# Kernel optimization log

Measured on AMD Instinct MI355X. Metric: run time of the kernel, lower is better.

## Reference

```python
import jax, jax.numpy as jnp
import numpy as np

BN_EPS = 1e-5

def _gin_mlp(h, wa, ba, wb, bb):
    # 2-layer MLP: Linear -> ReLU -> Linear
    return jax.nn.relu(h @ wa + ba) @ wb + bb

def _gin_conv(x, src, dst, n, wa, ba, wb, bb):
    # GIN aggregation: (1+eps)*x + sum_{j->i} x_j, eps=0 (PyG default)
    agg = jax.ops.segment_sum(x[src], dst, num_segments=n)
    return _gin_mlp(x + agg, wa, ba, wb, bb)

def _batchnorm(h, gamma, beta):
    # track_running_stats=False -> always batch stats, biased variance
    mean = jnp.mean(h, axis=0)
    var = jnp.var(h, axis=0)
    return (h - mean) * jax.lax.rsqrt(var + BN_EPS) * gamma + beta

def setup_inputs() -> dict:
    key = jax.random.key(0)
    ks = jax.random.split(key, 8)
    N, E, F, H, C = 100000, 1600000, 64, 64, 10
    s = 0.05
    return {
        "x": jax.random.normal(ks[0], (N, F), dtype=jnp.float32),
        "edge_index": jax.random.randint(ks[1], (2, E), 0, N, dtype=jnp.int64),
        "w1a": jax.random.normal(ks[2], (F, H), dtype=jnp.float32) * s,
        "b1a": jnp.zeros((H,), jnp.float32),
        "w1b": jax.random.normal(ks[3], (H, H), dtype=jnp.float32) * s,
        "b1b": jnp.zeros((H,), jnp.float32),
        "bn_gamma": jnp.ones((H,), jnp.float32),
        "bn_beta": jnp.zeros((H,), jnp.float32),
        "w2a": jax.random.normal(ks[4], (H, H), dtype=jnp.float32) * s,
        "b2a": jnp.zeros((H,), jnp.float32),
        "w2b": jax.random.normal(ks[5], (H, H), dtype=jnp.float32) * s,
        "b2b": jnp.zeros((H,), jnp.float32),
        "lin_w": jax.random.normal(ks[6], (H, C), dtype=jnp.float32) * s,
        "lin_b": jnp.zeros((C,), jnp.float32),
    }

def reference(x, edge_index, w1a, b1a, w1b, b1b, bn_gamma, bn_beta,
              w2a, b2a, w2b, b2b, lin_w, lin_b):
    n = x.shape[0]
    src, dst = edge_index[0], edge_index[1]
    h1 = _gin_conv(x, src, dst, n, w1a, b1a, w1b, b1b)   # [N, H]
    h1 = _batchnorm(h1, bn_gamma, bn_beta)               # relu1 never applied (faithful)
    h2 = _gin_conv(h1, src, dst, n, w2a, b2a, w2b, b2b)  # [N, H]
    return h2 @ lin_w + lin_b                            # [N, C]
```

## Files before the change

kernel.cpp:

```cpp
#include <hip/hip_runtime.h>
#include <hip/hip_fp16.h>

#define H 64
#define CBS 512
#define CB_BITS 9
#define TILE 8192
#define CAP 9216
#define NSTAT 64

typedef _Float16 f16;
typedef __attribute__((ext_vector_type(8))) _Float16 v8h;
typedef __attribute__((ext_vector_type(4))) float v4f;

__global__ __launch_bounds__(256)
void cvt_init_kernel(const float* __restrict__ x, f16* __restrict__ xh, int total4,
                     int* __restrict__ gcursor, int CB) {
    int i = blockIdx.x * blockDim.x + threadIdx.x;
    if (blockIdx.x == 0) {
        int t = threadIdx.x;
        if (t < CB) gcursor[t * 16] = t * CAP;
    }
    if (i >= total4) return;
    float4 v = ((const float4*)x)[i];
    f16 h0 = (f16)v.x, h1 = (f16)v.y, h2 = (f16)v.z, h3 = (f16)v.w;
    ushort4 pk;
    pk.x = *(unsigned short*)&h0; pk.y = *(unsigned short*)&h1;
    pk.z = *(unsigned short*)&h2; pk.w = *(unsigned short*)&h3;
    ((ushort4*)xh)[i] = pk;
}

__global__ __launch_bounds__(256)
void part_staged_kernel(const int* __restrict__ ei, int* __restrict__ gcursor,
                        int* __restrict__ pairs, int E, int N, int CB) {
    __shared__ int sd[256];
    __shared__ int excl[256];
    __shared__ int gbase[256];
    __shared__ int lcur[256];
    __shared__ int stage[TILE];
    __shared__ unsigned char bin8[TILE];
    int t = threadIdx.x;
    int ntiles = (E + TILE - 1) / TILE;
    for (int tile = blockIdx.x; tile < ntiles; tile += gridDim.x) {
        int base = tile * TILE;
        int cnt = min(TILE, E - base);
        sd[t] = 0;
        __syncthreads();
        for (int i = t; i < cnt; i += 256) {
            int s = ei[base + i];
            int d = ei[E + base + i];
            if ((unsigned)s < (unsigned)N && (unsigned)d < (unsigned)N)
                atomicAdd(&sd[d >> CB_BITS], 1);
        }
        __syncthreads();
        int v = sd[t];
        __syncthreads();
        for (int off = 1; off < 256; off <<= 1) {
            int add = (t >= off) ? sd[t - off] : 0;
            __syncthreads();
            sd[t] += add;
            __syncthreads();
        }
        int ex = sd[t] - v;
        excl[t] = ex;
        lcur[t] = ex;
        if (t < CB && v > 0) gbase[t] = atomicAdd(&gcursor[t * 16], v);
        int tot = sd[255];
        __syncthreads();
        for (int i = t; i < cnt; i += 256) {
            int s = ei[base + i];
            int d = ei[E + base + i];
            if ((unsigned)s < (unsigned)N && (unsigned)d < (unsigned)N) {
                int cb = d >> CB_BITS;
                int pos = atomicAdd(&lcur[cb], 1);
                stage[pos] = s | ((d & (CBS - 1)) << 17);
                bin8[pos] = (unsigned char)cb;
            }
        }
        __syncthreads();
        for (int i = t; i < tot; i += 256) {
            int b8 = bin8[i];
            pairs[gbase[b8] + (i - excl[b8])] = stage[i];
        }
        __syncthreads();
    }
}

__global__ __launch_bounds__(256)
void scan_cb_kernel(const int* __restrict__ gcursor, int* __restrict__ gbb,
                    int* __restrict__ rowptr, int CB, int N) {
    __shared__ int sd[256];
    int t = threadIdx.x;
    int cnt = (t < CB) ? (gcursor[t * 16] - t * CAP) : 0;
    sd[t] = cnt; __syncthreads();
    for (int off = 1; off < 256; off <<= 1) {
        int add = (t >= off) ? sd[t - off] : 0;
        __syncthreads();
        sd[t] += add;
        __syncthreads();
    }
    if (t < CB) gbb[t] = sd[t] - cnt;
    if (t == 0) { gbb[CB] = sd[255]; rowptr[N] = sd[255]; }
}

__global__ __launch_bounds__(256)
void bucket_csr_kernel(const int* __restrict__ pairs, const int* __restrict__ gcursor,
                       const int* __restrict__ gbb,
                       int* __restrict__ ebuf, int* __restrict__ rowptr, int N) {
    __shared__ int hist[CBS];
    __shared__ int cur[CBS];
    __shared__ int sd[256];
    __shared__ int carry_s;
    int b = blockIdx.x;
    int t = threadIdx.x;
    int pb = b * CAP;
    int cnt = gcursor[b * 16] - pb;
    int gb = gbb[b];
    for (int i = t; i < CBS; i += 256) hist[i] = 0;
    if (t == 0) carry_s = 0;
    __syncthreads();
    for (int i = t; i < cnt; i += 256)
        atomicAdd(&hist[(pairs[pb + i] >> 17) & (CBS - 1)], 1);
    __syncthreads();
    for (int start = 0; start < CBS; start += 256) {
        int v = hist[start + t];
        sd[t] = v; __syncthreads();
        for (int off = 1; off < 256; off <<= 1) {
            int add = (t >= off) ? sd[t - off] : 0;
            __syncthreads();
            sd[t] += add;
            __syncthreads();
        }
        int ex = sd[t] - v + carry_s;
        cur[start + t] = ex;
        int node = b * CBS + start + t;
        if (node < N) rowptr[node] = gb + ex;
        __syncthreads();
        if (t == 0) carry_s += sd[255];
        __syncthreads();
    }
    for (int i = t; i < cnt; i += 256) {
        int p = pairs[pb + i];
        int pos = atomicAdd(&cur[(p >> 17) & (CBS - 1)], 1);
        ebuf[gb + pos] = p & 0x1FFFF;
    }
}

__global__ void repack_kernel(const float* __restrict__ W1a, const float* __restrict__ W1b,
                              const float* __restrict__ W2a, const float* __restrict__ W2b,
                              const float* __restrict__ B2b, const float* __restrict__ LW,
                              const float* __restrict__ LB,
                              f16* __restrict__ pk1a, f16* __restrict__ pk1b,
                              f16* __restrict__ pk2a, f16* __restrict__ pkf,
                              float* __restrict__ bf, float* __restrict__ statsR) {
    int t = blockIdx.x * blockDim.x + threadIdx.x;
    if (t < NSTAT * 128) statsR[t] = 0.f;
    if (t < 12288) {
        int m = t >> 12;
        int e = t & 4095;
        int j = e & 7, lane = (e >> 3) & 63, ks = (e >> 9) & 1, nt = e >> 10;
        int row = ks * 32 + ((lane >> 4) & 3) * 8 + j;
        int col = nt * 16 + (lane & 15);
        const float* W = (m == 0) ? W1a : (m == 1) ? W1b : W2a;
        f16* P = (m == 0) ? pk1a : (m == 1) ? pk1b : pk2a;
        P[e] = (f16)W[row * 64 + col];
    } else if (t < 13312) {
        int e = t - 12288;
        int j = e & 7, lane = (e >> 3) & 63, ks = e >> 9;
        int row = ks * 32 + ((lane >> 4) & 3) * 8 + j;
        int col = lane & 15;
        float a = 0.f;
        if (col < 10)
            for (int m = 0; m < H; ++m) a = fmaf(W2b[row * 64 + m], LW[m * 10 + col], a);
        pkf[e] = (f16)a;
    } else if (t < 13322) {
        int c = t - 13312;
        float a = LB[c];
        for (int m = 0; m < H; ++m) a = fmaf(B2b[m], LW[m * 10 + c], a);
        bf[c] = a;
    }
}

__global__ __launch_bounds__(256)
void gather1_kernel(const f16* __restrict__ xh, const int* __restrict__ rowptr,
                    const int* __restrict__ ebuf, f16* __restrict__ bufA,
                    int N, int Em1) {
    int wid = (int)(((long long)blockIdx.x * blockDim.x + threadIdx.x) >> 6);
    int lane = threadIdx.x & 63;
    int g = lane >> 3, fl = lane & 7;
    int node = wid * 8 + g;
    bool vn = node < N;
    int p0 = 0, deg = 0;
    if (vn) {
        p0 = rowptr[node];
        deg = rowptr[node + 1] - p0;
    }
    int m = deg;
    m = max(m, __shfl_xor(m, 8));
    m = max(m, __shfl_xor(m, 16));
    m = max(m, __shfl_xor(m, 32));

    float a[8];
    {
        v8h s = {};
        if (vn) s = *(const v8h*)(xh + ((size_t)node << 6) + fl * 8);
#pragma unroll
        for (int j = 0; j < 8; ++j) a[j] = (float)s[j];
    }
    for (int k = 0; k < m; k += 4) {
        int idx[4];
#pragma unroll
        for (int q = 0; q < 4; ++q)
            idx[q] = ebuf[min(p0 + k + q, Em1)];
#pragma unroll
        for (int q = 0; q < 4; ++q) {
            if (k + q < deg) {
                v8h v = *(const v8h*)(xh + ((size_t)idx[q] << 6) + fl * 8);
#pragma unroll
                for (int j = 0; j < 8; ++j) a[j] += (float)v[j];
            }
        }
    }
    if (vn) {
        v8h o;
#pragma unroll
        for (int j = 0; j < 8; ++j) o[j] = (f16)a[j];
        *(v8h*)(bufA + ((size_t)node << 6) + fl * 8) = o;
    }
}

__global__ __launch_bounds__(256)
void gather2_kernel(const f16* __restrict__ h1p, const float* __restrict__ scale,
                    const float* __restrict__ shiftv, const int* __restrict__ rowptr,
                    const int* __restrict__ ebuf, f16* __restrict__ bufC,
                    int N, int Em1) {
    int wid = (int)(((long long)blockIdx.x * blockDim.x + threadIdx.x) >> 6);
    int lane = threadIdx.x & 63;
    int g = lane >> 3, fl = lane & 7;
    int node = wid * 8 + g;
    bool vn = node < N;
    int p0 = 0, deg = 0;
    if (vn) {
        p0 = rowptr[node];
        deg = rowptr[node + 1] - p0;
    }
    int m = deg;
    m = max(m, __shfl_xor(m, 8));
    m = max(m, __shfl_xor(m, 16));
    m = max(m, __shfl_xor(m, 32));

    float a[8];
    {
        v8h s = {};
        if (vn) s = *(const v8h*)(h1p + ((size_t)node << 6) + fl * 8);
#pragma unroll
        for (int j = 0; j < 8; ++j) a[j] = (float)s[j];
    }
    for (int k = 0; k < m; k += 4) {
        int idx[4];
#pragma unroll
        for (int q = 0; q < 4; ++q)
            idx[q] = ebuf[min(p0 + k + q, Em1)];
#pragma unroll
        for (int q = 0; q < 4; ++q) {
            if (k + q < deg) {
                v8h v = *(const v8h*)(h1p + ((size_t)idx[q] << 6) + fl * 8);
#pragma unroll
                for (int j = 0; j < 8; ++j) a[j] += (float)v[j];
            }
        }
    }
    if (vn) {
        float4 sc0 = *(const float4*)(scale + fl * 8);
        float4 sc1 = *(const float4*)(scale + fl * 8 + 4);
        float4 sh0 = *(const float4*)(shiftv + fl * 8);
        float4 sh1 = *(const float4*)(shiftv + fl * 8 + 4);
        float degp1 = (float)(deg + 1);
        float sc[8] = {sc0.x, sc0.y, sc0.z, sc0.w, sc1.x, sc1.y, sc1.z, sc1.w};
        float sh[8] = {sh0.x, sh0.y, sh0.z, sh0.w, sh1.x, sh1.y, sh1.z, sh1.w};
        v8h o;
#pragma unroll
        for (int j = 0; j < 8; ++j) o[j] = (f16)(a[j] * sc[j] + degp1 * sh[j]);
        *(v8h*)(bufC + ((size_t)node << 6) + fl * 8) = o;
    }
}

__global__ __launch_bounds__(256)
void mlp1_kernel(const f16* __restrict__ bufA, f16* __restrict__ h1p,
                 const f16* __restrict__ pk1a, const f16* __restrict__ pk1b,
                 const float* __restrict__ B1a, const float* __restrict__ B1b,
                 float* __restrict__ statsR, int N) {
    __shared__ f16 Su[4][16 * 72];
    __shared__ f16 Sh[4][16 * 72];
    __shared__ float red[2][4][64];
    int t = threadIdx.x, wv = t >> 6, lane = t & 63;
    int quad = lane >> 4, r16 = lane & 15;
    int node0 = blockIdx.x * 64 + wv * 16;
    int nodeA = node0 + r16;

    v8h a0 = {}, a1 = {};
    if (nodeA < N) {
        a0 = *(const v8h*)(bufA + (size_t)nodeA * 64 + quad * 8);
        a1 = *(const v8h*)(bufA + (size_t)nodeA * 64 + 32 + quad * 8);
    }
#pragma unroll
    for (int nt = 0; nt < 4; ++nt) {
        v8h b0 = *(const v8h*)(pk1a + (((nt * 2 + 0) * 64 + lane) << 3));
        v8h b1 = *(const v8h*)(pk1a + (((nt * 2 + 1) * 64 + lane) << 3));
        v4f c = {0.f, 0.f, 0.f, 0.f};
        c = __builtin_amdgcn_mfma_f32_16x16x32_f16(a0, b0, c, 0, 0, 0);
        c = __builtin_amdgcn_mfma_f32_16x16x32_f16(a1, b1, c, 0, 0, 0);
        float bias = B1a[nt * 16 + r16];
#pragma unroll
        for (int reg = 0; reg < 4; ++reg)
            Su[wv][(quad * 4 + reg) * 72 + nt * 16 + r16] = (f16)fmaxf(c[reg] + bias, 0.f);
    }
    __syncthreads();
    v8h u0 = *(const v8h*)(&Su[wv][r16 * 72 + quad * 8]);
    v8h u1 = *(const v8h*)(&Su[wv][r16 * 72 + 32 + quad * 8]);
#pragma unroll
    for (int nt = 0; nt < 4; ++nt) {
        v8h b0 = *(const v8h*)(pk1b + (((nt * 2 + 0) * 64 + lane) << 3));
        v8h b1 = *(const v8h*)(pk1b + (((nt * 2 + 1) * 64 + lane) << 3));
        v4f c = {0.f, 0.f, 0.f, 0.f};
        c = __builtin_amdgcn_mfma_f32_16x16x32_f16(u0, b0, c, 0, 0, 0);
        c = __builtin_amdgcn_mfma_f32_16x16x32_f16(u1, b1, c, 0, 0, 0);
        float bias = B1b[nt * 16 + r16];
#pragma unroll
        for (int reg = 0; reg < 4; ++reg) {
            int row = quad * 4 + reg;
            bool valid = (node0 + row) < N;
            Sh[wv][row * 72 + nt * 16 + r16] = valid ? (f16)(c[reg] + bias) : (f16)0;
        }
    }
    __syncthreads();
    for (int i = lane; i < 1024; i += 64) {
        int row = i >> 6, col = i & 63;
        int node = node0 + row;
        if (node < N) h1p[(size_t)node * 64 + col] = Sh[wv][row * 72 + col];
    }
    float s = 0.f, s2 = 0.f;
#pragma unroll
    for (int row = 0; row < 16; ++row) {
        float v = (float)Sh[wv][row * 72 + lane];
        s += v;
        s2 = fmaf(v, v, s2);
    }
    red[0][wv][lane] = s;
    red[1][wv][lane] = s2;
    __syncthreads();
    if (wv == 0) {
        float ts  = (red[0][0][lane] + red[0][1][lane]) + (red[0][2][lane] + red[0][3][lane]);
        float ts2 = (red[1][0][lane] + red[1][1][lane]) + (red[1][2][lane] + red[1][3][lane]);
        float* st = statsR + (size_t)(blockIdx.x & (NSTAT - 1)) * 128;
        unsafeAtomicAdd(&st[lane], ts);
        unsafeAtomicAdd(&st[64 + lane], ts2);
    }
}

__global__ void bn_finalize_kernel(const float* __restrict__ statsR,
                                   const float* __restrict__ gamma,
                                   const float* __restrict__ beta,
                                   float* __restrict__ scale, float* __restrict__ shiftv, float n) {
    int f = threadIdx.x;
    if (f >= H) return;
    float s = 0.f, s2 = 0.f;
    for (int r = 0; r < NSTAT; ++r) {
        s  += statsR[r * 128 + f];
        s2 += statsR[r * 128 + 64 + f];
    }
    float mean = s / n;
    float var = s2 / n - mean * mean;
    var = fmaxf(var, 0.f);
    float sc = gamma[f] * rsqrtf(var + 1e-5f);
    scale[f] = sc;
    shiftv[f] = beta[f] - mean * sc;
}

__global__ __launch_bounds__(256)
void mlp2_kernel(const f16* __restrict__ bufC,
                 const f16* __restrict__ pk2a, const f16* __restrict__ pkf,
                 const float* __restrict__ B2a, const float* __restrict__ bf,
                 float* __restrict__ out, int N) {
    __shared__ f16 Su[4][16 * 72];
    int t = threadIdx.x, wv = t >> 6, lane = t & 63;
    int quad = lane >> 4, r16 = lane & 15;
    int node0 = blockIdx.x * 64 + wv * 16;
    int nodeA = node0 + r16;

    v8h a0 = {}, a1 = {};
    if (nodeA < N) {
        a0 = *(const v8h*)(bufC + (size_t)nodeA * 64 + quad * 8);
        a1 = *(const v8h*)(bufC + (size_t)nodeA * 64 + 32 + quad * 8);
    }
#pragma unroll
    for (int nt = 0; nt < 4; ++nt) {
        v8h b0 = *(const v8h*)(pk2a + (((nt * 2 + 0) * 64 + lane) << 3));
        v8h b1 = *(const v8h*)(pk2a + (((nt * 2 + 1) * 64 + lane) << 3));
        v4f c = {0.f, 0.f, 0.f, 0.f};
        c = __builtin_amdgcn_mfma_f32_16x16x32_f16(a0, b0, c, 0, 0, 0);
        c = __builtin_amdgcn_mfma_f32_16x16x32_f16(a1, b1, c, 0, 0, 0);
        float bias = B2a[nt * 16 + r16];
#pragma unroll
        for (int reg = 0; reg < 4; ++reg)
            Su[wv][(quad * 4 + reg) * 72 + nt * 16 + r16] = (f16)fmaxf(c[reg] + bias, 0.f);
    }
    __syncthreads();
    v8h u0 = *(const v8h*)(&Su[wv][r16 * 72 + quad * 8]);
    v8h u1 = *(const v8h*)(&Su[wv][r16 * 72 + 32 + quad * 8]);
    v8h b0 = *(const v8h*)(pkf + ((0 * 64 + lane) << 3));
    v8h b1 = *(const v8h*)(pkf + ((1 * 64 + lane) << 3));
    v4f c = {0.f, 0.f, 0.f, 0.f};
    c = __builtin_amdgcn_mfma_f32_16x16x32_f16(u0, b0, c, 0, 0, 0);
    c = __builtin_amdgcn_mfma_f32_16x16x32_f16(u1, b1, c, 0, 0, 0);
    if (r16 < 10) {
        float bias = bf[r16];
#pragma unroll
        for (int reg = 0; reg < 4; ++reg) {
            int node = node0 + quad * 4 + reg;
            if (node < N) out[(size_t)node * 10 + r16] = c[reg] + bias;
        }
    }
}

extern "C" void kernel_launch(void* const* d_in, const int* in_sizes, int n_in,
                              void* d_out, int out_size, void* d_ws, size_t ws_size,
                              hipStream_t stream) {
    const float* x    = (const float*)d_in[0];
    const int*   ei   = (const int*)d_in[1];
    const float* w1a  = (const float*)d_in[2];
    const float* b1a  = (const float*)d_in[3];
    const float* w1b  = (const float*)d_in[4];
    const float* b1b  = (const float*)d_in[5];
    const float* bng  = (const float*)d_in[6];
    const float* bnb  = (const float*)d_in[7];
    const float* w2a  = (const float*)d_in[8];
    const float* b2a  = (const float*)d_in[9];
    const float* w2b  = (const float*)d_in[10];
    const float* b2b  = (const float*)d_in[11];
    const float* linw = (const float*)d_in[12];
    const float* linb = (const float*)d_in[13];

    int N = in_sizes[0] / H;
    int E = in_sizes[1] / 2;
    int CB = (N + CBS - 1) / CBS;

    size_t NH = (size_t)N * H;
    char*  wsb    = (char*)d_ws;
    f16*   xh     = (f16*)wsb;
    f16*   bufA   = (f16*)(wsb + NH * 2);
    f16*   bufC   = (f16*)(wsb + NH * 4);
    float* stats  = (float*)(wsb + NH * 6);
    float* scale  = stats + 128;
    float* shiftv = stats + 192;
    float* bf     = stats + 256;
    f16*   pk1a   = (f16*)(bf + 16);
    f16*   pk1b   = pk1a + 4096;
    f16*   pk2a   = pk1b + 4096;
    f16*   pkf    = pk2a + 4096;
    int*   gcursor= (int*)(pkf + 1024);
    int*   gbb    = gcursor + 256 * 16;
    int*   rowptr = gbb + 257;
    int*   ebuf   = rowptr + (N + 1);
    int*   pairs  = ebuf + E;
    float* statsR = (float*)pairs;

    int ntiles = (E + TILE - 1) / TILE;

    cvt_init_kernel<<<(int)((NH / 4 + 255) / 256), 256, 0, stream>>>(
        x, xh, (int)(NH / 4), gcursor, CB);
    part_staged_kernel<<<ntiles, 256, 0, stream>>>(ei, gcursor, pairs, E, N, CB);
    scan_cb_kernel<<<1, 256, 0, stream>>>(gcursor, gbb, rowptr, CB, N);
    bucket_csr_kernel<<<CB, 256, 0, stream>>>(pairs, gcursor, gbb, ebuf, rowptr, N);
    repack_kernel<<<(13322 + 255) / 256, 256, 0, stream>>>(
        w1a, w1b, w2a, w2b, b2b, linw, linb, pk1a, pk1b, pk2a, pkf, bf, statsR);

    int nwaves = (N + 7) / 8;
    int gblocks = (int)(((long long)nwaves * 64 + 255) / 256);
    int mblocks = (N + 63) / 64;
    gather1_kernel<<<gblocks, 256, 0, stream>>>(xh, rowptr, ebuf, bufA, N, E - 1);
    mlp1_kernel<<<mblocks, 256, 0, stream>>>(bufA, bufA, pk1a, pk1b, b1a, b1b, statsR, N);
    bn_finalize_kernel<<<1, 64, 0, stream>>>(statsR, bng, bnb, scale, shiftv, (float)N);

    gather2_kernel<<<gblocks, 256, 0, stream>>>(bufA, scale, shiftv, rowptr, ebuf, bufC, N, E - 1);
    mlp2_kernel<<<mblocks, 256, 0, stream>>>(bufC, pk2a, pkf, b2a, bf, (float*)d_out, N);
}
```

Baseline: 247.9 us.

## Fuse gathers into MLP kernels and merge front-end preprocessing kernels

Each neighbor-aggregation gather is fused into its following MFMA MLP kernel, so aggregated features stay in shared memory instead of going through a global buffer. The fp16 conversion, edge partitioning and weight repacking become one front kernel with block-range dispatch, and the bucket-count scan moves into every bucket_csr block. This removes several launches and a full N×64 write and read per layer. In exchange the fused kernels use more shared memory and registers, which may lower occupancy for the latency-bound gathers, and the scan is repeated in every block.

```diff
diff --git a/kernel.cpp b/kernel.cpp
--- a/kernel.cpp
+++ b/kernel.cpp
@@ -7,41 +7,41 @@
 #define TILE 8192
 #define CAP 9216
 #define NSTAT 64
+#define RPK_BLKS 53
 
 typedef _Float16 f16;
 typedef __attribute__((ext_vector_type(8))) _Float16 v8h;
 typedef __attribute__((ext_vector_type(4))) float v4f;
 
 __global__ __launch_bounds__(256)
-void cvt_init_kernel(const float* __restrict__ x, f16* __restrict__ xh, int total4,
-                     int* __restrict__ gcursor, int CB) {
-    int i = blockIdx.x * blockDim.x + threadIdx.x;
-    if (blockIdx.x == 0) {
-        int t = threadIdx.x;
-        if (t < CB) gcursor[t * 16] = t * CAP;
-    }
-    if (i >= total4) return;
-    float4 v = ((const float4*)x)[i];
-    f16 h0 = (f16)v.x, h1 = (f16)v.y, h2 = (f16)v.z, h3 = (f16)v.w;
-    ushort4 pk;
-    pk.x = *(unsigned short*)&h0; pk.y = *(unsigned short*)&h1;
-    pk.z = *(unsigned short*)&h2; pk.w = *(unsigned short*)&h3;
-    ((ushort4*)xh)[i] = pk;
+void init_kernel(int* __restrict__ gcursor, float* __restrict__ statsR, int CB) {
+    int t = threadIdx.x;
+    if (t < CB) gcursor[t * 16] = t * CAP;
+    for (int i = t; i < NSTAT * 128; i += 256) statsR[i] = 0.f;
 }
 
 __global__ __launch_bounds__(256)
-void part_staged_kernel(const int* __restrict__ ei, int* __restrict__ gcursor,
-                        int* __restrict__ pairs, int E, int N, int CB) {
+void front_kernel(const int* __restrict__ ei, int* __restrict__ gcursor,
+                  int* __restrict__ pairs, int E, int N, int CB, int ntiles,
+                  const float* __restrict__ x, f16* __restrict__ xh, int total4,
+                  const float* __restrict__ W1a, const float* __restrict__ W1b,
+                  const float* __restrict__ W2a, const float* __restrict__ W2b,
+                  const float* __restrict__ B2b, const float* __restrict__ LW,
+                  const float* __restrict__ LB,
+                  f16* __restrict__ pk1a, f16* __restrict__ pk1b,
+                  f16* __restrict__ pk2a, f16* __restrict__ pkf,
+                  float* __restrict__ bf) {
     __shared__ int sd[256];
     __shared__ int excl[256];
     __shared__ int gbase[256];
     __shared__ int lcur[256];
     __shared__ int stage[TILE];
     __shared__ unsigned char bin8[TILE];
+    int b = blockIdx.x;
     int t = threadIdx.x;
-    int ntiles = (E + TILE - 1) / TILE;
-    for (int tile = blockIdx.x; tile < ntiles; tile += gridDim.x) {
-        int base = tile * TILE;
+
+    if (b < ntiles) {
+        int base = b * TILE;
         int cnt = min(TILE, E - base);
         sd[t] = 0;
         __syncthreads();
@@ -81,40 +81,71 @@
             int b8 = bin8[i];
             pairs[gbase[b8] + (i - excl[b8])] = stage[i];
         }
-        __syncthreads();
-    }
-}
-
-__global__ __launch_bounds__(256)
-void scan_cb_kernel(const int* __restrict__ gcursor, int* __restrict__ gbb,
-                    int* __restrict__ rowptr, int CB, int N) {
-    __shared__ int sd[256];
-    int t = threadIdx.x;
-    int cnt = (t < CB) ? (gcursor[t * 16] - t * CAP) : 0;
-    sd[t] = cnt; __syncthreads();
-    for (int off = 1; off < 256; off <<= 1) {
-        int add = (t >= off) ? sd[t - off] : 0;
-        __syncthreads();
-        sd[t] += add;
-        __syncthreads();
-    }
-    if (t < CB) gbb[t] = sd[t] - cnt;
-    if (t == 0) { gbb[CB] = sd[255]; rowptr[N] = sd[255]; }
+        return;
+    }
+    b -= ntiles;
+    if (b < RPK_BLKS) {
+        int tt = b * 256 + t;
+        if (tt < 12288) {
+            int m = tt >> 12;
+            int e = tt & 4095;
+            int j = e & 7, lane = (e >> 3) & 63, ks = (e >> 9) & 1, nt = e >> 10;
+            int row = ks * 32 + ((lane >> 4) & 3) * 8 + j;
+            int col = nt * 16 + (lane & 15);
+            const float* W = (m == 0) ? W1a : (m == 1) ? W1b : W2a;
+            f16* P = (m == 0) ? pk1a : (m == 1) ? pk1b : pk2a;
+            P[e] = (f16)W[row * 64 + col];
+        } else if (tt < 13312) {
+            int e = tt - 12288;
+            int j = e & 7, lane = (e >> 3) & 63, ks = e >> 9;
+            int row = ks * 32 + ((lane >> 4) & 3) * 8 + j;
+            int col = lane & 15;
+            float a = 0.f;
+            if (col < 10)
+                for (int m = 0; m < H; ++m) a = fmaf(W2b[row * 64 + m], LW[m * 10 + col], a);
+            pkf[e] = (f16)a;
+        } else if (tt < 13322) {
+            int c = tt - 13312;
+            float a = LB[c];
+            for (int m = 0; m < H; ++m) a = fmaf(B2b[m], LW[m * 10 + c], a);
+            bf[c] = a;
+        }
+        return;
+    }
+    b -= RPK_BLKS;
+    int i = b * 256 + t;
+    if (i >= total4) return;
+    float4 v = ((const float4*)x)[i];
+    f16 h0 = (f16)v.x, h1 = (f16)v.y, h2 = (f16)v.z, h3 = (f16)v.w;
+    ushort4 pk;
+    pk.x = *(unsigned short*)&h0; pk.y = *(unsigned short*)&h1;
+    pk.z = *(unsigned short*)&h2; pk.w = *(unsigned short*)&h3;
+    ((ushort4*)xh)[i] = pk;
 }
 
 __global__ __launch_bounds__(256)
 void bucket_csr_kernel(const int* __restrict__ pairs, const int* __restrict__ gcursor,
-                       const int* __restrict__ gbb,
-                       int* __restrict__ ebuf, int* __restrict__ rowptr, int N) {
+                       int* __restrict__ ebuf, int* __restrict__ rowptr, int N, int CB) {
     __shared__ int hist[CBS];
     __shared__ int cur[CBS];
     __shared__ int sd[256];
     __shared__ int carry_s;
     int b = blockIdx.x;
     int t = threadIdx.x;
+    int c_t = (t < CB) ? (gcursor[t * 16] - t * CAP) : 0;
+    sd[t] = c_t; __syncthreads();
+    for (int off = 1; off < 256; off <<= 1) {
+        int add = (t >= off) ? sd[t - off] : 0;
+        __syncthreads();
+        sd[t] += add;
+        __syncthreads();
+    }
+    int cnt = gcursor[b * 16] - b * CAP;
+    int gb = sd[b] - cnt;
+    if (b == 0 && t == 0) rowptr[N] = sd[255];
+    __syncthreads();
+
     int pb = b * CAP;
-    int cnt = gcursor[b * 16] - pb;
-    int gb = gbb[b];
     for (int i = t; i < CBS; i += 256) hist[i] = 0;
     if (t == 0) carry_s = 0;
     __syncthreads();
@@ -145,163 +176,66 @@
     }
 }
 
-__global__ void repack_kernel(const float* __restrict__ W1a, const float* __restrict__ W1b,
-                              const float* __restrict__ W2a, const float* __restrict__ W2b,
-                              const float* __restrict__ B2b, const float* __restrict__ LW,
-                              const float* __restrict__ LB,
-                              f16* __restrict__ pk1a, f16* __restrict__ pk1b,
-                              f16* __restrict__ pk2a, f16* __restrict__ pkf,
-                              float* __restrict__ bf, float* __restrict__ statsR) {
-    int t = blockIdx.x * blockDim.x + threadIdx.x;
-    if (t < NSTAT * 128) statsR[t] = 0.f;
-    if (t < 12288) {
-        int m = t >> 12;
-        int e = t & 4095;
-        int j = e & 7, lane = (e >> 3) & 63, ks = (e >> 9) & 1, nt = e >> 10;
-        int row = ks * 32 + ((lane >> 4) & 3) * 8 + j;
-        int col = nt * 16 + (lane & 15);
-        const float* W = (m == 0) ? W1a : (m == 1) ? W1b : W2a;
-        f16* P = (m == 0) ? pk1a : (m == 1) ? pk1b : pk2a;
-        P[e] = (f16)W[row * 64 + col];
-    } else if (t < 13312) {
-        int e = t - 12288;
-        int j = e & 7, lane = (e >> 3) & 63, ks = e >> 9;
-        int row = ks * 32 + ((lane >> 4) & 3) * 8 + j;
-        int col = lane & 15;
-        float a = 0.f;
-        if (col < 10)
-            for (int m = 0; m < H; ++m) a = fmaf(W2b[row * 64 + m], LW[m * 10 + col], a);
-        pkf[e] = (f16)a;
-    } else if (t < 13322) {
-        int c = t - 13312;
-        float a = LB[c];
-        for (int m = 0; m < H; ++m) a = fmaf(B2b[m], LW[m * 10 + c], a);
-        bf[c] = a;
-    }
-}
-
 __global__ __launch_bounds__(256)
-void gather1_kernel(const f16* __restrict__ xh, const int* __restrict__ rowptr,
-                    const int* __restrict__ ebuf, f16* __restrict__ bufA,
-                    int N, int Em1) {
-    int wid = (int)(((long long)blockIdx.x * blockDim.x + threadIdx.x) >> 6);
-    int lane = threadIdx.x & 63;
-    int g = lane >> 3, fl = lane & 7;
-    int node = wid * 8 + g;
-    bool vn = node < N;
-    int p0 = 0, deg = 0;
-    if (vn) {
-        p0 = rowptr[node];
-        deg = rowptr[node + 1] - p0;
-    }
-    int m = deg;
-    m = max(m, __shfl_xor(m, 8));
-    m = max(m, __shfl_xor(m, 16));
-    m = max(m, __shfl_xor(m, 32));
-
-    float a[8];
-    {
-        v8h s = {};
-        if (vn) s = *(const v8h*)(xh + ((size_t)node << 6) + fl * 8);
-#pragma unroll
-        for (int j = 0; j < 8; ++j) a[j] = (float)s[j];
-    }
-    for (int k = 0; k < m; k += 4) {
-        int idx[4];
-#pragma unroll
-        for (int q = 0; q < 4; ++q)
-            idx[q] = ebuf[min(p0 + k + q, Em1)];
-#pragma unroll
-        for (int q = 0; q < 4; ++q) {
-            if (k + q < deg) {
-                v8h v = *(const v8h*)(xh + ((size_t)idx[q] << 6) + fl * 8);
-#pragma unroll
-                for (int j = 0; j < 8; ++j) a[j] += (float)v[j];
-            }
-        }
-    }
-    if (vn) {
-        v8h o;
-#pragma unroll
-        for (int j = 0; j < 8; ++j) o[j] = (f16)a[j];
-        *(v8h*)(bufA + ((size_t)node << 6) + fl * 8) = o;
-    }
-}
-
-__global__ __launch_bounds__(256)
-void gather2_kernel(const f16* __restrict__ h1p, const float* __restrict__ scale,
-                    const float* __restrict__ shiftv, const int* __restrict__ rowptr,
-                    const int* __restrict__ ebuf, f16* __restrict__ bufC,
-                    int N, int Em1) {
-    int wid = (int)(((long long)blockIdx.x * blockDim.x + threadIdx.x) >> 6);
-    int lane = threadIdx.x & 63;
-    int g = lane >> 3, fl = lane & 7;
-    int node = wid * 8 + g;
-    bool vn = node < N;
-    int p0 = 0, deg = 0;
-    if (vn) {
-        p0 = rowptr[node];
-        deg = rowptr[node + 1] - p0;
-    }
-    int m = deg;
-    m = max(m, __shfl_xor(m, 8));
-    m = max(m, __shfl_xor(m, 16));
-    m = max(m, __shfl_xor(m, 32));
-
-    float a[8];
-    {
-        v8h s = {};
-        if (vn) s = *(const v8h*)(h1p + ((size_t)node << 6) + fl * 8);
-#pragma unroll
-        for (int j = 0; j < 8; ++j) a[j] = (float)s[j];
-    }
-    for (int k = 0; k < m; k += 4) {
-        int idx[4];
-#pragma unroll
-        for (int q = 0; q < 4; ++q)
-            idx[q] = ebuf[min(p0 + k + q, Em1)];
-#pragma unroll
-        for (int q = 0; q < 4; ++q) {
-            if (k + q < deg) {
-                v8h v = *(const v8h*)(h1p + ((size_t)idx[q] << 6) + fl * 8);
-#pragma unroll
-                for (int j = 0; j < 8; ++j) a[j] += (float)v[j];
-            }
-        }
-    }
-    if (vn) {
-        float4 sc0 = *(const float4*)(scale + fl * 8);
-        float4 sc1 = *(const float4*)(scale + fl * 8 + 4);
-        float4 sh0 = *(const float4*)(shiftv + fl * 8);
-        float4 sh1 = *(const float4*)(shiftv + fl * 8 + 4);
-        float degp1 = (float)(deg + 1);
-        float sc[8] = {sc0.x, sc0.y, sc0.z, sc0.w, sc1.x, sc1.y, sc1.z, sc1.w};
-        float sh[8] = {sh0.x, sh0.y, sh0.z, sh0.w, sh1.x, sh1.y, sh1.z, sh1.w};
-        v8h o;
-#pragma unroll
-        for (int j = 0; j < 8; ++j) o[j] = (f16)(a[j] * sc[j] + degp1 * sh[j]);
-        *(v8h*)(bufC + ((size_t)node << 6) + fl * 8) = o;
-    }
-}
-
-__global__ __launch_bounds__(256)
-void mlp1_kernel(const f16* __restrict__ bufA, f16* __restrict__ h1p,
-                 const f16* __restrict__ pk1a, const f16* __restrict__ pk1b,
-                 const float* __restrict__ B1a, const float* __restrict__ B1b,
-                 float* __restrict__ statsR, int N) {
+void g1mlp1_kernel(const f16* __restrict__ xh, const int* __restrict__ rowptr,
+                   const int* __restrict__ ebuf, f16* __restrict__ h1p,
+                   const f16* __restrict__ pk1a, const f16* __restrict__ pk1b,
+                   const float* __restrict__ B1a, const float* __restrict__ B1b,
+                   float* __restrict__ statsR, int N, int Em1) {
+    __shared__ f16 agg[64][72];
     __shared__ f16 Su[4][16 * 72];
     __shared__ f16 Sh[4][16 * 72];
     __shared__ float red[2][4][64];
     int t = threadIdx.x, wv = t >> 6, lane = t & 63;
+    int g = lane >> 3, fl = lane & 7;
+    int node0 = blockIdx.x * 64;
+
+#pragma unroll
+    for (int r = 0; r < 2; ++r) {
+        int nl = wv * 16 + r * 8 + g;
+        int node = node0 + nl;
+        bool vn = node < N;
+        int p0 = 0, deg = 0;
+        if (vn) {
+            p0 = rowptr[node];
+            deg = rowptr[node + 1] - p0;
+        }
+        int m = deg;
+        m = max(m, __shfl_xor(m, 8));
+        m = max(m, __shfl_xor(m, 16));
+        m = max(m, __shfl_xor(m, 32));
+        float a[8];
+        {
+            v8h s = {};
+            if (vn) s = *(const v8h*)(xh + ((size_t)node << 6) + fl * 8);
+#pragma unroll
+            for (int j = 0; j < 8; ++j) a[j] = (float)s[j];
+        }
+        for (int k = 0; k < m; k += 4) {
+            int idx[4];
+#pragma unroll
+            for (int q = 0; q < 4; ++q)
+                idx[q] = ebuf[min(p0 + k + q, Em1)];
+#pragma unroll
+            for (int q = 0; q < 4; ++q) {
+                if (k + q < deg) {
+                    v8h v = *(const v8h*)(xh + ((size_t)idx[q] << 6) + fl * 8);
+#pragma unroll
+                    for (int j = 0; j < 8; ++j) a[j] += (float)v[j];
+                }
+            }
+        }
+        v8h o;
+#pragma unroll
+        for (int j = 0; j < 8; ++j) o[j] = (f16)a[j];
+        *(v8h*)(&agg[nl][fl * 8]) = o;
+    }
+    __syncthreads();
+
     int quad = lane >> 4, r16 = lane & 15;
-    int node0 = blockIdx.x * 64 + wv * 16;
-    int nodeA = node0 + r16;
-
-    v8h a0 = {}, a1 = {};
-    if (nodeA < N) {
-        a0 = *(const v8h*)(bufA + (size_t)nodeA * 64 + quad * 8);
-        a1 = *(const v8h*)(bufA + (size_t)nodeA * 64 + 32 + quad * 8);
-    }
+    int nodeA_l = wv * 16 + r16;
+    v8h a0 = *(const v8h*)(&agg[nodeA_l][quad * 8]);
+    v8h a1 = *(const v8h*)(&agg[nodeA_l][32 + quad * 8]);
 #pragma unroll
     for (int nt = 0; nt < 4; ++nt) {
         v8h b0 = *(const v8h*)(pk1a + (((nt * 2 + 0) * 64 + lane) << 3));
@@ -328,14 +262,15 @@
 #pragma unroll
         for (int reg = 0; reg < 4; ++reg) {
             int row = quad * 4 + reg;
-            bool valid = (node0 + row) < N;
+            bool valid = (node0 + wv * 16 + row) < N;
             Sh[wv][row * 72 + nt * 16 + r16] = valid ? (f16)(c[reg] + bias) : (f16)0;
         }
     }
     __syncthreads();
+    int nbase = node0 + wv * 16;
     for (int i = lane; i < 1024; i += 64) {
         int row = i >> 6, col = i & 63;
-        int node = node0 + row;
+        int node = nbase + row;
         if (node < N) h1p[(size_t)node * 64 + col] = Sh[wv][row * 72 + col];
     }
     float s = 0.f, s2 = 0.f;
@@ -377,21 +312,77 @@
 }
 
 __global__ __launch_bounds__(256)
-void mlp2_kernel(const f16* __restrict__ bufC,
-                 const f16* __restrict__ pk2a, const f16* __restrict__ pkf,
-                 const float* __restrict__ B2a, const float* __restrict__ bf,
-                 float* __restrict__ out, int N) {
+void g2mlp2_kernel(const f16* __restrict__ h1p, const float* __restrict__ scale,
+                   const float* __restrict__ shiftv, const int* __restrict__ rowptr,
+                   const int* __restrict__ ebuf,
+                   const f16* __restrict__ pk2a, const f16* __restrict__ pkf,
+                   const float* __restrict__ B2a, const float* __restrict__ bf,
+                   float* __restrict__ out, int N, int Em1) {
+    __shared__ f16 agg[64][72];
     __shared__ f16 Su[4][16 * 72];
     int t = threadIdx.x, wv = t >> 6, lane = t & 63;
+    int g = lane >> 3, fl = lane & 7;
+    int node0 = blockIdx.x * 64;
+
+    float sc[8], sh[8];
+    {
+        float4 s0 = *(const float4*)(scale + fl * 8);
+        float4 s1 = *(const float4*)(scale + fl * 8 + 4);
+        float4 h0 = *(const float4*)(shiftv + fl * 8);
+        float4 h1 = *(const float4*)(shiftv + fl * 8 + 4);
+        sc[0]=s0.x; sc[1]=s0.y; sc[2]=s0.z; sc[3]=s0.w;
+        sc[4]=s1.x; sc[5]=s1.y; sc[6]=s1.z; sc[7]=s1.w;
+        sh[0]=h0.x; sh[1]=h0.y; sh[2]=h0.z; sh[3]=h0.w;
+        sh[4]=h1.x; sh[5]=h1.y; sh[6]=h1.z; sh[7]=h1.w;
+    }
+
+#pragma unroll
+    for (int r = 0; r < 2; ++r) {
+        int nl = wv * 16 + r * 8 + g;
+        int node = node0 + nl;
+        bool vn = node < N;
+        int p0 = 0, deg = 0;
+        if (vn) {
+            p0 = rowptr[node];
+            deg = rowptr[node + 1] - p0;
+        }
+        int m = deg;
+        m = max(m, __shfl_xor(m, 8));
+        m = max(m, __shfl_xor(m, 16));
+        m = max(m, __shfl_xor(m, 32));
+        float a[8];
+        {
+            v8h s = {};
+            if (vn) s = *(const v8h*)(h1p + ((size_t)node << 6) + fl * 8);
+#pragma unroll
+            for (int j = 0; j < 8; ++j) a[j] = (float)s[j];
+        }
+        for (int k = 0; k < m; k += 4) {
+            int idx[4];
+#pragma unroll
+            for (int q = 0; q < 4; ++q)
+                idx[q] = ebuf[min(p0 + k + q, Em1)];
+#pragma unroll
+            for (int q = 0; q < 4; ++q) {
+                if (k + q < deg) {
+                    v8h v = *(const v8h*)(h1p + ((size_t)idx[q] << 6) + fl * 8);
+#pragma unroll
+                    for (int j = 0; j < 8; ++j) a[j] += (float)v[j];
+                }
+            }
+        }
+        float degp1 = (float)(deg + 1);
+        v8h o;
+#pragma unroll
+        for (int j = 0; j < 8; ++j) o[j] = (f16)(a[j] * sc[j] + degp1 * sh[j]);
+        *(v8h*)(&agg[nl][fl * 8]) = o;
+    }
+    __syncthreads();
+
     int quad = lane >> 4, r16 = lane & 15;
-    int node0 = blockIdx.x * 64 + wv * 16;
-    int nodeA = node0 + r16;
-
-    v8h a0 = {}, a1 = {};
-    if (nodeA < N) {
-        a0 = *(const v8h*)(bufC + (size_t)nodeA * 64 + quad * 8);
-        a1 = *(const v8h*)(bufC + (size_t)nodeA * 64 + 32 + quad * 8);
-    }
+    int nodeA_l = wv * 16 + r16;
+    v8h a0 = *(const v8h*)(&agg[nodeA_l][quad * 8]);
+    v8h a1 = *(const v8h*)(&agg[nodeA_l][32 + quad * 8]);
 #pragma unroll
     for (int nt = 0; nt < 4; ++nt) {
         v8h b0 = *(const v8h*)(pk2a + (((nt * 2 + 0) * 64 + lane) << 3));
@@ -416,7 +407,7 @@
         float bias = bf[r16];
 #pragma unroll
         for (int reg = 0; reg < 4; ++reg) {
-            int node = node0 + quad * 4 + reg;
+            int node = node0 + wv * 16 + quad * 4 + reg;
             if (node < N) out[(size_t)node * 10 + r16] = c[reg] + bias;
         }
     }
@@ -447,8 +438,7 @@
     size_t NH = (size_t)N * H;
     char*  wsb    = (char*)d_ws;
     f16*   xh     = (f16*)wsb;
-    f16*   bufA   = (f16*)(wsb + NH * 2);
-    f16*   bufC   = (f16*)(wsb + NH * 4);
+    f16*   h1p    = (f16*)(wsb + NH * 2);
     float* stats  = (float*)(wsb + NH * 6);
     float* scale  = stats + 128;
     float* shiftv = stats + 192;
@@ -458,29 +448,26 @@
     f16*   pk2a   = pk1b + 4096;
     f16*   pkf    = pk2a + 4096;
     int*   gcursor= (int*)(pkf + 1024);
-    int*   gbb    = gcursor + 256 * 16;
-    int*   rowptr = gbb + 257;
+    int*   rowptr = gcursor + 256 * 16;
     int*   ebuf   = rowptr + (N + 1);
     int*   pairs  = ebuf + E;
-    float* statsR = (float*)pairs;
+    float* statsR = (float*)(pairs + (size_t)CB * CAP);
 
     int ntiles = (E + TILE - 1) / TILE;
-
-    cvt_init_kernel<<<(int)((NH / 4 + 255) / 256), 256, 0, stream>>>(
-        x, xh, (int)(NH / 4), gcursor, CB);
-    part_staged_kernel<<<ntiles, 256, 0, stream>>>(ei, gcursor, pairs, E, N, CB);
-    scan_cb_kernel<<<1, 256, 0, stream>>>(gcursor, gbb, rowptr, CB, N);
-    bucket_csr_kernel<<<CB, 256, 0, stream>>>(pairs, gcursor, gbb, ebuf, rowptr, N);
-    repack_kernel<<<(13322 + 255) / 256, 256, 0, stream>>>(
-        w1a, w1b, w2a, w2b, b2b, linw, linb, pk1a, pk1b, pk2a, pkf, bf, statsR);
-
-    int nwaves = (N + 7) / 8;
-    int gblocks = (int)(((long long)nwaves * 64 + 255) / 256);
+    int total4 = (int)(NH / 4);
+    int cvtblocks = (total4 + 255) / 256;
     int mblocks = (N + 63) / 64;
-    gather1_kernel<<<gblocks, 256, 0, stream>>>(xh, rowptr, ebuf, bufA, N, E - 1);
-    mlp1_kernel<<<mblocks, 256, 0, stream>>>(bufA, bufA, pk1a, pk1b, b1a, b1b, statsR, N);
+
+    init_kernel<<<1, 256, 0, stream>>>(gcursor, statsR, CB);
+    front_kernel<<<ntiles + RPK_BLKS + cvtblocks, 256, 0, stream>>>(
+        ei, gcursor, pairs, E, N, CB, ntiles,
+        x, xh, total4,
+        w1a, w1b, w2a, w2b, b2b, linw, linb,
+        pk1a, pk1b, pk2a, pkf, bf);
+    bucket_csr_kernel<<<CB, 256, 0, stream>>>(pairs, gcursor, ebuf, rowptr, N, CB);
+    g1mlp1_kernel<<<mblocks, 256, 0, stream>>>(
+        xh, rowptr, ebuf, h1p, pk1a, pk1b, b1a, b1b, statsR, N, E - 1);
     bn_finalize_kernel<<<1, 64, 0, stream>>>(statsR, bng, bnb, scale, shiftv, (float)N);
-
-    gather2_kernel<<<gblocks, 256, 0, stream>>>(bufA, scale, shiftv, rowptr, ebuf, bufC, N, E - 1);
-    mlp2_kernel<<<mblocks, 256, 0, stream>>>(bufC, pk2a, pkf, b2a, bf, (float*)d_out, N);
-}
+    g2mlp2_kernel<<<mblocks, 256, 0, stream>>>(
+        h1p, scale, shiftv, rowptr, ebuf, pk2a, pkf, b2a, bf, (float*)d_out, N, E - 1);
+}
```

Result: no change. 246.1 us (-0.7%).
